# Optimization experiments

Measured on AMD Instinct MI355X. Metric: run time of the kernel, lower is better.

Reference implementation:

```python
import jax, jax.numpy as jnp
import numpy as np

# ----- problem dimensions (must match setup_inputs) -----
B = 50          # graphs per batch
NPG = 2000      # nodes per graph (equal-size graphs)
N = B * NPG     # total nodes = 100_000
D = 128         # in_channels
E = 600_000     # total edges
EA = 16         # edge_attr_dim
RATIO = 0.5
K = int(RATIO * NPG)  # nodes kept per graph = 1000
EPS = 1e-6


def setup_inputs() -> dict:
    key = jax.random.key(0)
    ks = jax.random.split(key, 12)
    x = jax.random.normal(ks[0], (N, D), jnp.float32)
    # edges constrained within graphs (each graph owns a contiguous node block)
    eg = jax.random.randint(ks[1], (E,), 0, B)
    src = eg * NPG + jax.random.randint(ks[2], (E,), 0, NPG)
    dst = eg * NPG + jax.random.randint(ks[3], (E,), 0, NPG)
    edge_index = jnp.stack([src, dst]).astype(jnp.int32)
    edge_attr = jax.random.normal(ks[4], (E, EA), jnp.float32)
    batch = (jnp.arange(N) // NPG).astype(jnp.int32)
    # feat_mlp: Linear(D,D) -> ReLU -> Linear(D,1)
    W1 = jax.random.normal(ks[5], (D, D), jnp.float32) / np.sqrt(D)
    b1 = jnp.zeros((D,), jnp.float32)
    W2 = jax.random.normal(ks[6], (D, 1), jnp.float32) / np.sqrt(D)
    b2 = jnp.zeros((1,), jnp.float32)
    # edge_mlp: Linear(EA,D) -> ReLU -> Linear(D,1)
    We1 = jax.random.normal(ks[7], (EA, D), jnp.float32) / np.sqrt(EA)
    be1 = jnp.zeros((D,), jnp.float32)
    We2 = jax.random.normal(ks[8], (D, 1), jnp.float32) / np.sqrt(D)
    be2 = jnp.zeros((1,), jnp.float32)
    view_weight = jnp.ones((3,), jnp.float32)
    return {"x": x, "edge_index": edge_index, "edge_attr": edge_attr,
            "batch": batch, "W1": W1, "b1": b1, "W2": W2, "b2": b2,
            "We1": We1, "be1": be1, "We2": We2, "be2": be2,
            "view_weight": view_weight}


def _standardize(v):
    # torch .std() is unbiased (ddof=1)
    return (v - v.mean()) / (jnp.std(v, ddof=1) + EPS)


def _scores(x, src, dst, edge_attr, W1, b1, W2, b2, We1, be1, We2, be2, vw):
    # edge weights: softplus(edge_mlp(edge_attr)) + eps
    ew = jax.nn.softplus((jax.nn.relu(edge_attr @ We1 + be1) @ We2 + be2)[:, 0]) + EPS
    deg_w = jnp.zeros((N,), x.dtype).at[src].add(ew)
    dis = jnp.where(deg_w > 0, deg_w ** -0.5, 0.0)
    norm = dis[src] * ew * dis[dst]                       # [E]
    x_diff = jnp.zeros_like(x).at[src].add(x[dst] * norm[:, None])  # [N,D]
    # view 1: structural (log degree)
    deg_c = jnp.zeros((N,), x.dtype).at[src].add(1.0)
    struct_score = _standardize(jnp.log(deg_c + 1.0))
    # view 2: feature MLP
    feat_raw = (jax.nn.relu(x @ W1 + b1) @ W2 + b2)[:, 0]
    feat_score = _standardize(feat_raw)
    # view 3: diffusion cosine similarity
    dot = jnp.sum(x * x_diff, axis=-1)
    cos = dot / ((jnp.linalg.norm(x, axis=-1) + EPS) *
                 (jnp.linalg.norm(x_diff, axis=-1) + EPS))
    diff_score = _standardize(cos)
    raw = jnp.stack([struct_score, feat_score, diff_score], axis=-1) @ vw
    return jax.nn.sigmoid(raw)                            # [N]


def reference(x, edge_index, edge_attr, batch, W1, b1, W2, b2,
              We1, be1, We2, be2, view_weight):
    src, dst = edge_index[0], edge_index[1]
    score = _scores(x, src, dst, edge_attr, W1, b1, W2, b2,
                    We1, be1, We2, be2, view_weight)
    # vectorized per-graph top-k (graphs are equal-size contiguous blocks)
    loc = jax.lax.top_k(score.reshape(B, NPG), K)[1]      # [B,K] local indices
    keep = (jnp.arange(B, dtype=loc.dtype)[:, None] * NPG + loc).reshape(-1)  # [B*K]
    node_mask = jnp.zeros((N,), bool).at[keep].set(True)
    new_id = jnp.full((N,), -1, jnp.int32).at[keep].set(
        jnp.arange(B * K, dtype=jnp.int32))
    e_mask = node_mask[src] & node_mask[dst]              # [E]
    out_edge_index = jnp.where(e_mask[None, :],
                               jnp.stack([new_id[src], new_id[dst]]), 0)
    out_edge_attr = jnp.where(e_mask[:, None], edge_attr, 0.0)
    out_x = x[keep] * score[keep][:, None]                # [B*K, D]
    out_batch = (jnp.arange(B * K) // K).astype(batch.dtype)
    return out_x, out_edge_index, out_edge_attr, out_batch, e_mask
```

## Files before the change

kernel.cpp:

```cpp
#include <hip/hip_runtime.h>
#include <math.h>

#define NN   100000
#define DD   128
#define EE   600000
#define EAD  16
#define BB   50
#define NPG  2000
#define KK   1000
#define NKEEP (BB*KK)

#define OFF_OEI    6400000
#define OFF_OEA    7600000
#define OFF_OBATCH 17200000
#define OFF_EMASK  17250000

#define NRED 240
#define SCAN_NB 98

__global__ __launch_bounds__(256) void k_edge_mlp(
    const float* __restrict__ edge_attr, const int* __restrict__ src,
    const float* __restrict__ We1, const float* __restrict__ be1,
    const float* __restrict__ We2, const float* __restrict__ be2,
    float* __restrict__ ew, float* __restrict__ deg_w, float* __restrict__ deg_c)
{
    int e = blockIdx.x * 256 + threadIdx.x;
    if (e >= EE) return;
    const float4* ap = (const float4*)(edge_attr + (size_t)e * EAD);
    float4 a0 = ap[0], a1 = ap[1], a2 = ap[2], a3 = ap[3];
    float ea[16] = {a0.x,a0.y,a0.z,a0.w, a1.x,a1.y,a1.z,a1.w,
                    a2.x,a2.y,a2.z,a2.w, a3.x,a3.y,a3.z,a3.w};
    float acc = be2[0];
    for (int j = 0; j < DD; j++) {
        float h = be1[j];
        #pragma unroll
        for (int k = 0; k < 16; k++) h += ea[k] * We1[k*DD + j];
        acc += fmaxf(h, 0.f) * We2[j];
    }
    float sp = fmaxf(acc, 0.f) + log1pf(expf(-fabsf(acc)));
    float w = sp + 1e-6f;
    ew[e] = w;
    int s = src[e];
    atomicAdd(&deg_w[s], w);
    atomicAdd(&deg_c[s], 1.0f);
}

__global__ __launch_bounds__(256) void k_dis(const float* __restrict__ deg_w,
                                             float* __restrict__ dis)
{
    int n = blockIdx.x * 256 + threadIdx.x;
    if (n >= NN) return;
    float d = deg_w[n];
    dis[n] = d > 0.f ? 1.f / sqrtf(d) : 0.f;
}

__global__ __launch_bounds__(1024) void k_scan_block(
    const float* __restrict__ deg_c, int* __restrict__ scanned,
    int* __restrict__ blocksums)
{
    __shared__ int s[1024];
    int i = blockIdx.x * 1024 + threadIdx.x;
    int c = (i < NN) ? (int)deg_c[i] : 0;
    s[threadIdx.x] = c;
    __syncthreads();
    for (int off = 1; off < 1024; off <<= 1) {
        int v = (threadIdx.x >= off) ? s[threadIdx.x - off] : 0;
        __syncthreads();
        s[threadIdx.x] += v;
        __syncthreads();
    }
    if (i < NN) scanned[i] = s[threadIdx.x] - c;
    if (threadIdx.x == 1023) blocksums[blockIdx.x] = s[1023];
}

__global__ __launch_bounds__(128) void k_scan_top(int* __restrict__ blocksums)
{
    __shared__ int s[128];
    int c = (threadIdx.x < SCAN_NB) ? blocksums[threadIdx.x] : 0;
    s[threadIdx.x] = c;
    __syncthreads();
    for (int off = 1; off < 128; off <<= 1) {
        int v = (threadIdx.x >= off) ? s[threadIdx.x - off] : 0;
        __syncthreads();
        s[threadIdx.x] += v;
        __syncthreads();
    }
    if (threadIdx.x < SCAN_NB) blocksums[threadIdx.x] = s[threadIdx.x] - c;
}

__global__ __launch_bounds__(256) void k_cursor(
    const int* __restrict__ scanned, const int* __restrict__ blocksums,
    int* __restrict__ rowstart, int* __restrict__ cur)
{
    int n = blockIdx.x * 256 + threadIdx.x;
    if (n >= NN) return;
    int st = scanned[n] + blocksums[n >> 10];
    rowstart[n] = st;
    cur[n] = st;
}

__global__ __launch_bounds__(256) void k_scatter(
    const int* __restrict__ src, const int* __restrict__ dst,
    const float* __restrict__ ew, const float* __restrict__ dis,
    int* __restrict__ cur, int* __restrict__ csr_dst, float* __restrict__ csr_w)
{
    int e = blockIdx.x * 256 + threadIdx.x;
    if (e >= EE) return;
    int s = src[e], d = dst[e];
    float w = dis[s] * ew[e] * dis[d];
    int pos = atomicAdd(&cur[s], 1);
    csr_dst[pos] = d;
    csr_w[pos] = w;
}

__global__ __launch_bounds__(256) void k_gather(
    const int* __restrict__ rowstart, const float* __restrict__ deg_c,
    const int* __restrict__ csr_dst, const float* __restrict__ csr_w,
    const float* __restrict__ x, float* __restrict__ x_diff)
{
    int wid = (blockIdx.x * 256 + threadIdx.x) >> 6;
    int lane = threadIdx.x & 63;
    if (wid >= NN) return;
    int start = rowstart[wid];
    int end = start + (int)deg_c[wid];
    const float2* xp = (const float2*)x;
    float2 acc = {0.f, 0.f};
    for (int e = start; e < end; e++) {
        int d = csr_dst[e];
        float w = csr_w[e];
        float2 xv = xp[(size_t)d * 64 + lane];
        acc.x += xv.x * w;
        acc.y += xv.y * w;
    }
    ((float2*)x_diff)[(size_t)wid * 64 + lane] = acc;
}

__global__ __launch_bounds__(256) void k_node(
    const float* __restrict__ x, const float* __restrict__ x_diff,
    const float* __restrict__ W1, const float* __restrict__ b1,
    const float* __restrict__ W2, const float* __restrict__ b2,
    const float* __restrict__ deg_c,
    float* __restrict__ raw0, float* __restrict__ raw1, float* __restrict__ raw2)
{
    __shared__ float xs[32 * DD];
    int wave = threadIdx.x >> 6, lane = threadIdx.x & 63;
    int nodeBase = blockIdx.x * 32 + wave * 8;

    const float4* xp = (const float4*)(x + (size_t)nodeBase * DD);
    float4* sp4 = (float4*)(xs + wave * 1024);
    #pragma unroll
    for (int i = 0; i < 4; i++) sp4[lane + 64*i] = xp[lane + 64*i];
    __syncthreads();

    const float* xw = xs + wave * 1024;
    float acc[8], acc2[8];
    float b1a = b1[lane], b1b = b1[lane + 64];
    #pragma unroll
    for (int i = 0; i < 8; i++) { acc[i] = b1a; acc2[i] = b1b; }

    for (int k = 0; k < DD; k += 4) {
        float w1a[4], w1b[4];
        #pragma unroll
        for (int kk = 0; kk < 4; kk++) {
            w1a[kk] = W1[(k+kk)*DD + lane];
            w1b[kk] = W1[(k+kk)*DD + lane + 64];
        }
        #pragma unroll
        for (int i = 0; i < 8; i++) {
            float4 xv = *(const float4*)(xw + i*DD + k);
            acc[i]  += xv.x*w1a[0]; acc[i]  += xv.y*w1a[1];
            acc[i]  += xv.z*w1a[2]; acc[i]  += xv.w*w1a[3];
            acc2[i] += xv.x*w1b[0]; acc2[i] += xv.y*w1b[1];
            acc2[i] += xv.z*w1b[2]; acc2[i] += xv.w*w1b[3];
        }
    }
    float w2a = W2[lane], w2b = W2[lane + 64];
    #pragma unroll
    for (int i = 0; i < 8; i++) {
        float v = fmaxf(acc[i], 0.f) * w2a + fmaxf(acc2[i], 0.f) * w2b;
        #pragma unroll
        for (int off = 32; off; off >>= 1) v += __shfl_xor(v, off, 64);
        if (lane == 0) raw1[nodeBase + i] = v + b2[0];
    }
    #pragma unroll
    for (int i = 0; i < 8; i++) {
        int n = nodeBase + i;
        float x1 = xw[i*DD + lane], x2 = xw[i*DD + lane + 64];
        float d1 = x_diff[(size_t)n*DD + lane], d2 = x_diff[(size_t)n*DD + lane + 64];
        float dot = x1*d1 + x2*d2;
        float nx  = x1*x1 + x2*x2;
        float nd  = d1*d1 + d2*d2;
        #pragma unroll
        for (int off = 32; off; off >>= 1) {
            dot += __shfl_xor(dot, off, 64);
            nx  += __shfl_xor(nx,  off, 64);
            nd  += __shfl_xor(nd,  off, 64);
        }
        if (lane == 0)
            raw2[n] = dot / ((sqrtf(nx) + 1e-6f) * (sqrtf(nd) + 1e-6f));
    }
    if (lane < 8) {
        int n = nodeBase + lane;
        raw0[n] = logf(deg_c[n] + 1.0f);
    }
}

__global__ __launch_bounds__(256) void k_reduce(
    const float* __restrict__ r0, const float* __restrict__ r1,
    const float* __restrict__ r2, double* __restrict__ partials)
{
    __shared__ double sd[256];
    double s[6] = {0,0,0,0,0,0};
    for (int n = blockIdx.x * 256 + threadIdx.x; n < NN; n += 256 * NRED) {
        double v0 = r0[n], v1 = r1[n], v2 = r2[n];
        s[0] += v0; s[1] += v0*v0;
        s[2] += v1; s[3] += v1*v1;
        s[4] += v2; s[5] += v2*v2;
    }
    for (int q = 0; q < 6; q++) {
        sd[threadIdx.x] = s[q];
        __syncthreads();
        for (int off = 128; off; off >>= 1) {
            if (threadIdx.x < off) sd[threadIdx.x] += sd[threadIdx.x + off];
            __syncthreads();
        }
        if (threadIdx.x == 0) partials[blockIdx.x * 6 + q] = sd[0];
        __syncthreads();
    }
}

__global__ __launch_bounds__(256) void k_stats(const double* __restrict__ partials,
                                               float* __restrict__ stats)
{
    __shared__ double sd[256];
    __shared__ double sums[6];
    for (int q = 0; q < 6; q++) {
        sd[threadIdx.x] = (threadIdx.x < NRED) ? partials[threadIdx.x * 6 + q] : 0.0;
        __syncthreads();
        for (int off = 128; off; off >>= 1) {
            if (threadIdx.x < off) sd[threadIdx.x] += sd[threadIdx.x + off];
            __syncthreads();
        }
        if (threadIdx.x == 0) sums[q] = sd[0];
        __syncthreads();
    }
    if (threadIdx.x == 0) {
        for (int i = 0; i < 3; i++) {
            double sum = sums[2*i], sq = sums[2*i+1];
            double mean = sum / NN;
            double var = (sq - sum * sum / NN) / (NN - 1);
            double sdv = sqrt(var > 0 ? var : 0);
            stats[2*i]   = (float)mean;
            stats[2*i+1] = (float)(1.0 / (sdv + 1e-6));
        }
    }
}

__global__ __launch_bounds__(256) void k_score(
    const float* __restrict__ r0, const float* __restrict__ r1,
    const float* __restrict__ r2, const float* __restrict__ stats,
    const float* __restrict__ vw, float* __restrict__ score)
{
    int n = blockIdx.x * 256 + threadIdx.x;
    if (n >= NN) return;
    float z0 = (r0[n] - stats[0]) * stats[1];
    float z1 = (r1[n] - stats[2]) * stats[3];
    float z2 = (r2[n] - stats[4]) * stats[5];
    float r = z0 * vw[0] + z1 * vw[1] + z2 * vw[2];
    score[n] = 1.f / (1.f + expf(-r));
}

__global__ __launch_bounds__(1024) void k_topk(
    const float* __restrict__ score, int* __restrict__ keep,
    int* __restrict__ new_id, float* __restrict__ obatch)
{
    __shared__ unsigned long long keys[2048];
    int b = blockIdx.x;
    unsigned t = threadIdx.x;
    for (unsigned i = t; i < 2048; i += 1024) {
        unsigned long long kk = 0ull;
        if (i < NPG) {
            float sc = score[b * NPG + i];
            kk = ((unsigned long long)__float_as_uint(sc) << 32)
               | (unsigned long long)(0xFFFFFFFFu - i);
        }
        keys[i] = kk;
    }
    __syncthreads();
    for (unsigned k = 2; k <= 2048; k <<= 1) {
        for (unsigned j = k >> 1; j > 0; j >>= 1) {
            unsigned i = ((t & ~(j - 1)) << 1) | (t & (j - 1));
            unsigned p = i | j;
            unsigned long long a = keys[i], c = keys[p];
            bool up = ((i & k) == 0);
            if ((a < c) == up) { keys[i] = c; keys[p] = a; }
            __syncthreads();
        }
    }
    if (t < KK) {
        unsigned long long kk = keys[t];
        unsigned li = 0xFFFFFFFFu - (unsigned)(kk & 0xFFFFFFFFu);
        int node = b * NPG + (int)li;
        int j = b * KK + (int)t;
        keep[j] = node;
        new_id[node] = j;
        obatch[j] = (float)b;
    }
}

__global__ __launch_bounds__(128) void k_outx(
    const float* __restrict__ x, const float* __restrict__ score,
    const int* __restrict__ keep, float* __restrict__ out_x)
{
    int j = blockIdx.x;
    int node = keep[j];
    float s = score[node];
    out_x[(size_t)j * DD + threadIdx.x] = x[(size_t)node * DD + threadIdx.x] * s;
}

__global__ __launch_bounds__(256) void k_edges(
    const int* __restrict__ src, const int* __restrict__ dst,
    const int* __restrict__ new_id, float* __restrict__ oei,
    float* __restrict__ emask)
{
    int e = blockIdx.x * 256 + threadIdx.x;
    if (e >= EE) return;
    int ns = new_id[src[e]], nd = new_id[dst[e]];
    bool m = (ns >= 0) && (nd >= 0);
    oei[e]      = m ? (float)ns : 0.f;
    oei[EE + e] = m ? (float)nd : 0.f;
    emask[e]    = m ? 1.f : 0.f;
}

__global__ __launch_bounds__(256) void k_attr(
    const float* __restrict__ edge_attr, const float* __restrict__ emask,
    float* __restrict__ oea)
{
    int idx = blockIdx.x * 256 + threadIdx.x;
    if (idx >= EE * 4) return;
    int e = idx >> 2;
    float m = emask[e];
    float4 v = ((const float4*)edge_attr)[idx];
    float4 o; o.x = v.x*m; o.y = v.y*m; o.z = v.z*m; o.w = v.w*m;
    ((float4*)oea)[idx] = o;
}

extern "C" void kernel_launch(void* const* d_in, const int* in_sizes, int n_in,
                              void* d_out, int out_size, void* d_ws, size_t ws_size,
                              hipStream_t stream) {
    const float* x         = (const float*)d_in[0];
    const int*   edge_idx  = (const int*)d_in[1];
    const float* edge_attr = (const float*)d_in[2];
    const float* W1  = (const float*)d_in[4];
    const float* b1  = (const float*)d_in[5];
    const float* W2  = (const float*)d_in[6];
    const float* b2  = (const float*)d_in[7];
    const float* We1 = (const float*)d_in[8];
    const float* be1 = (const float*)d_in[9];
    const float* We2 = (const float*)d_in[10];
    const float* be2 = (const float*)d_in[11];
    const float* vw  = (const float*)d_in[12];

    const int* src = edge_idx;
    const int* dst = edge_idx + EE;

    float* out    = (float*)d_out;
    float* out_x  = out;
    float* oei    = out + OFF_OEI;
    float* oea    = out + OFF_OEA;
    float* obatch = out + OFF_OBATCH;
    float* emask  = out + OFF_EMASK;

    float* x_diff    = out;
    int*   csr_dst   = (int*)(out + 12800000);
    float* csr_w     = out + 13400000;
    int*   rowstart  = (int*)(out + 14000000);
    int*   cur       = (int*)(out + 14100000);
    int*   scanned   = (int*)(out + 14200000);
    int*   blocksums = (int*)(out + 14300000);

    float* ws     = (float*)d_ws;
    float* ew     = ws;
    float* deg_w  = ws + 600000;
    float* deg_c  = ws + 700000;
    float* dis    = ws + 800000;
    float* score  = ws + 900000;
    float* raw0   = ws + 1000000;
    float* raw1   = ws + 1100000;
    float* raw2   = ws + 1200000;
    int*   keep   = (int*)(ws + 1300000);
    int*   new_id = (int*)(ws + 1350000);
    double* partials = (double*)(ws + 1450000);
    float* stats  = ws + 1450000 + 2 * 6 * NRED;

    hipMemsetAsync(deg_w, 0, NN * sizeof(float), stream);
    hipMemsetAsync(deg_c, 0, NN * sizeof(float), stream);
    hipMemsetAsync(new_id, 0xFF, NN * sizeof(int), stream);

    k_edge_mlp<<<(EE + 255) / 256, 256, 0, stream>>>(edge_attr, src, We1, be1, We2, be2,
                                                     ew, deg_w, deg_c);
    k_dis<<<(NN + 255) / 256, 256, 0, stream>>>(deg_w, dis);
    k_scan_block<<<SCAN_NB, 1024, 0, stream>>>(deg_c, scanned, blocksums);
    k_scan_top<<<1, 128, 0, stream>>>(blocksums);
    k_cursor<<<(NN + 255) / 256, 256, 0, stream>>>(scanned, blocksums, rowstart, cur);
    k_scatter<<<(EE + 255) / 256, 256, 0, stream>>>(src, dst, ew, dis, cur, csr_dst, csr_w);
    k_gather<<<(NN * 64 + 255) / 256, 256, 0, stream>>>(rowstart, deg_c, csr_dst, csr_w,
                                                        x, x_diff);
    k_node<<<NN / 32, 256, 0, stream>>>(x, x_diff, W1, b1, W2, b2, deg_c,
                                        raw0, raw1, raw2);
    k_reduce<<<NRED, 256, 0, stream>>>(raw0, raw1, raw2, partials);
    k_stats<<<1, 256, 0, stream>>>(partials, stats);
    k_score<<<(NN + 255) / 256, 256, 0, stream>>>(raw0, raw1, raw2, stats, vw, score);
    k_topk<<<BB, 1024, 0, stream>>>(score, keep, new_id, obatch);
    k_outx<<<NKEEP, 128, 0, stream>>>(x, score, keep, out_x);
    k_edges<<<(EE + 255) / 256, 256, 0, stream>>>(src, dst, new_id, oei, emask);
    k_attr<<<(EE * 4 + 255) / 256, 256, 0, stream>>>(edge_attr, emask, oea);
}
```

Before: 511.1 us.

## Register-tile node MLP matmul as 4x8 per thread with padded shared memory

Restructures k_node so each block handles 64 nodes and each thread computes a 4-node by 8-output register tile of the first linear layer. W1 is read as float4 and reused across 4 nodes, and the shared-memory rows are padded to avoid bank conflicts. The two memsets for the adjacent deg_w and deg_c buffers are merged into one. This cuts redundant W1 loads per FMA at the cost of higher register pressure and more shared memory per block, which may lower occupancy.

```diff
diff --git a/kernel.cpp b/kernel.cpp
--- a/kernel.cpp
+++ b/kernel.cpp
@@ -135,6 +135,7 @@
     ((float2*)x_diff)[(size_t)wid * 64 + lane] = acc;
 }
 
+#define XSTR 132
 __global__ __launch_bounds__(256) void k_node(
     const float* __restrict__ x, const float* __restrict__ x_diff,
     const float* __restrict__ W1, const float* __restrict__ b1,
@@ -142,66 +143,97 @@
     const float* __restrict__ deg_c,
     float* __restrict__ raw0, float* __restrict__ raw1, float* __restrict__ raw2)
 {
-    __shared__ float xs[32 * DD];
+    __shared__ float xs[64 * XSTR];
     int wave = threadIdx.x >> 6, lane = threadIdx.x & 63;
-    int nodeBase = blockIdx.x * 32 + wave * 8;
-
-    const float4* xp = (const float4*)(x + (size_t)nodeBase * DD);
-    float4* sp4 = (float4*)(xs + wave * 1024);
+    int ng = lane >> 4, jg = lane & 15;
+    int blockBase = blockIdx.x * 64;
+
     #pragma unroll
-    for (int i = 0; i < 4; i++) sp4[lane + 64*i] = xp[lane + 64*i];
+    for (int it = 0; it < 8; it++) {
+        int s = threadIdx.x + 256 * it;
+        int row = s >> 5, c4 = s & 31;
+        int gn = blockBase + row; if (gn >= NN) gn = NN - 1;
+        *(float4*)(xs + row * XSTR + c4 * 4) =
+            *(const float4*)(x + (size_t)gn * DD + c4 * 4);
+    }
     __syncthreads();
 
-    const float* xw = xs + wave * 1024;
-    float acc[8], acc2[8];
-    float b1a = b1[lane], b1b = b1[lane + 64];
+    const float* xw = xs + (wave * 16 + ng * 4) * XSTR;
+    int j0 = jg * 8;
+    float acc[4][8];
     #pragma unroll
-    for (int i = 0; i < 8; i++) { acc[i] = b1a; acc2[i] = b1b; }
+    for (int i = 0; i < 4; i++)
+        #pragma unroll
+        for (int jj = 0; jj < 8; jj++) acc[i][jj] = 0.f;
 
     for (int k = 0; k < DD; k += 4) {
-        float w1a[4], w1b[4];
+        float4 xv[4];
+        #pragma unroll
+        for (int i = 0; i < 4; i++) xv[i] = *(const float4*)(xw + i * XSTR + k);
+        float4 wv[4][2];
         #pragma unroll
         for (int kk = 0; kk < 4; kk++) {
-            w1a[kk] = W1[(k+kk)*DD + lane];
-            w1b[kk] = W1[(k+kk)*DD + lane + 64];
-        }
-        #pragma unroll
-        for (int i = 0; i < 8; i++) {
-            float4 xv = *(const float4*)(xw + i*DD + k);
-            acc[i]  += xv.x*w1a[0]; acc[i]  += xv.y*w1a[1];
-            acc[i]  += xv.z*w1a[2]; acc[i]  += xv.w*w1a[3];
-            acc2[i] += xv.x*w1b[0]; acc2[i] += xv.y*w1b[1];
-            acc2[i] += xv.z*w1b[2]; acc2[i] += xv.w*w1b[3];
-        }
-    }
-    float w2a = W2[lane], w2b = W2[lane + 64];
+            wv[kk][0] = *(const float4*)(W1 + (k + kk) * DD + j0);
+            wv[kk][1] = *(const float4*)(W1 + (k + kk) * DD + j0 + 4);
+        }
+        #pragma unroll
+        for (int i = 0; i < 4; i++) {
+            const float xe[4] = {xv[i].x, xv[i].y, xv[i].z, xv[i].w};
+            #pragma unroll
+            for (int kk = 0; kk < 4; kk++) {
+                acc[i][0] += xe[kk] * wv[kk][0].x;
+                acc[i][1] += xe[kk] * wv[kk][0].y;
+                acc[i][2] += xe[kk] * wv[kk][0].z;
+                acc[i][3] += xe[kk] * wv[kk][0].w;
+                acc[i][4] += xe[kk] * wv[kk][1].x;
+                acc[i][5] += xe[kk] * wv[kk][1].y;
+                acc[i][6] += xe[kk] * wv[kk][1].z;
+                acc[i][7] += xe[kk] * wv[kk][1].w;
+            }
+        }
+    }
+
+    float4 b1a = *(const float4*)(b1 + j0), b1b = *(const float4*)(b1 + j0 + 4);
+    float4 w2a = *(const float4*)(W2 + j0), w2b = *(const float4*)(W2 + j0 + 4);
+    const float b1v[8] = {b1a.x,b1a.y,b1a.z,b1a.w, b1b.x,b1b.y,b1b.z,b1b.w};
+    const float w2v[8] = {w2a.x,w2a.y,w2a.z,w2a.w, w2b.x,w2b.y,w2b.z,w2b.w};
+    float bias2 = b2[0];
     #pragma unroll
-    for (int i = 0; i < 8; i++) {
-        float v = fmaxf(acc[i], 0.f) * w2a + fmaxf(acc2[i], 0.f) * w2b;
-        #pragma unroll
-        for (int off = 32; off; off >>= 1) v += __shfl_xor(v, off, 64);
-        if (lane == 0) raw1[nodeBase + i] = v + b2[0];
-    }
-    #pragma unroll
-    for (int i = 0; i < 8; i++) {
-        int n = nodeBase + i;
-        float x1 = xw[i*DD + lane], x2 = xw[i*DD + lane + 64];
-        float d1 = x_diff[(size_t)n*DD + lane], d2 = x_diff[(size_t)n*DD + lane + 64];
-        float dot = x1*d1 + x2*d2;
-        float nx  = x1*x1 + x2*x2;
-        float nd  = d1*d1 + d2*d2;
+    for (int i = 0; i < 4; i++) {
+        float p = 0.f;
+        #pragma unroll
+        for (int jj = 0; jj < 8; jj++)
+            p += fmaxf(acc[i][jj] + b1v[jj], 0.f) * w2v[jj];
+        p += __shfl_xor(p, 1, 64);
+        p += __shfl_xor(p, 2, 64);
+        p += __shfl_xor(p, 4, 64);
+        p += __shfl_xor(p, 8, 64);
+        int node = blockBase + wave * 16 + ng * 4 + i;
+        if (jg == 0 && node < NN) raw1[node] = p + bias2;
+    }
+
+    const float* xwv = xs + wave * 16 * XSTR;
+    #pragma unroll 1
+    for (int nd = 0; nd < 16; nd++) {
+        int node = blockBase + wave * 16 + nd;
+        int rn = node < NN ? node : NN - 1;
+        float2 xv2 = *(const float2*)(xwv + nd * XSTR + lane * 2);
+        float2 xd2 = *(const float2*)(x_diff + (size_t)rn * DD + lane * 2);
+        float dot = xv2.x * xd2.x + xv2.y * xd2.y;
+        float nx  = xv2.x * xv2.x + xv2.y * xv2.y;
+        float ndn = xd2.x * xd2.x + xd2.y * xd2.y;
         #pragma unroll
         for (int off = 32; off; off >>= 1) {
             dot += __shfl_xor(dot, off, 64);
             nx  += __shfl_xor(nx,  off, 64);
-            nd  += __shfl_xor(nd,  off, 64);
-        }
-        if (lane == 0)
-            raw2[n] = dot / ((sqrtf(nx) + 1e-6f) * (sqrtf(nd) + 1e-6f));
-    }
-    if (lane < 8) {
-        int n = nodeBase + lane;
-        raw0[n] = logf(deg_c[n] + 1.0f);
+            ndn += __shfl_xor(ndn, off, 64);
+        }
+        if (lane == 0 && node < NN)
+            raw2[node] = dot / ((sqrtf(nx) + 1e-6f) * (sqrtf(ndn) + 1e-6f));
+    }
+    if (lane < 16) {
+        int node = blockBase + wave * 16 + lane;
+        if (node < NN) raw0[node] = logf(deg_c[node] + 1.0f);
     }
 }
 
@@ -393,8 +425,7 @@
     double* partials = (double*)(ws + 1450000);
     float* stats  = ws + 1450000 + 2 * 6 * NRED;
 
-    hipMemsetAsync(deg_w, 0, NN * sizeof(float), stream);
-    hipMemsetAsync(deg_c, 0, NN * sizeof(float), stream);
+    hipMemsetAsync(deg_w, 0, 2 * NN * sizeof(float), stream);
     hipMemsetAsync(new_id, 0xFF, NN * sizeof(int), stream);
 
     k_edge_mlp<<<(EE + 255) / 256, 256, 0, stream>>>(edge_attr, src, We1, be1, We2, be2,
@@ -406,8 +437,8 @@
     k_scatter<<<(EE + 255) / 256, 256, 0, stream>>>(src, dst, ew, dis, cur, csr_dst, csr_w);
     k_gather<<<(NN * 64 + 255) / 256, 256, 0, stream>>>(rowstart, deg_c, csr_dst, csr_w,
                                                         x, x_diff);
-    k_node<<<NN / 32, 256, 0, stream>>>(x, x_diff, W1, b1, W2, b2, deg_c,
-                                        raw0, raw1, raw2);
+    k_node<<<(NN + 63) / 64, 256, 0, stream>>>(x, x_diff, W1, b1, W2, b2, deg_c,
+                                               raw0, raw1, raw2);
     k_reduce<<<NRED, 256, 0, stream>>>(raw0, raw1, raw2, partials);
     k_stats<<<1, 256, 0, stream>>>(partials, stats);
     k_score<<<(NN + 255) / 256, 256, 0, stream>>>(raw0, raw1, raw2, stats, vw, score);
```

Result: no change. 512.5 us (+0.3%).
